# Kernel tuning notes

Hardware: AMD Instinct MI355X
Metric: run time of the kernel (lower is better)

Reference implementation:

```python
import jax, jax.numpy as jnp
import numpy as np

N_NODES = 50000
N_EDGES = 800000
HID = 128
HEADS = 1
VOCAB = 1001  # input_dim + 1
OUT = 16
NEG_SLOPE = 0.2  # DGL GATv2Conv default


def setup_inputs():
    key = jax.random.key(0)
    ks = jax.random.split(key, 12)
    s = 1.0 / np.sqrt(HID)
    inp = {}
    inp['feats'] = jax.random.randint(ks[0], (N_NODES, 2), 0, VOCAB, dtype=jnp.int64)
    inp['src'] = jax.random.randint(ks[1], (N_EDGES,), 0, N_NODES, dtype=jnp.int32)
    inp['dst'] = jax.random.randint(ks[2], (N_EDGES,), 0, N_NODES, dtype=jnp.int32)
    inp['key_emb'] = jax.random.normal(ks[3], (VOCAB, HID), jnp.float32)
    inp['val_emb'] = jax.random.normal(ks[4], (VOCAB, HID), jnp.float32)
    inp['W1'] = jax.random.uniform(ks[5], (HID, HEADS * HID), jnp.float32, -s, s)
    inp['attn1'] = jax.random.uniform(ks[6], (HEADS, HID), jnp.float32, -s, s)
    inp['W2'] = jax.random.uniform(ks[7], (HID, HEADS * HID), jnp.float32, -s, s)
    inp['attn2'] = jax.random.uniform(ks[8], (HEADS, HID), jnp.float32, -s, s)
    inp['cls_w'] = jax.random.uniform(ks[9], (HID, OUT), jnp.float32, -s, s)
    return inp


def _gatv2_layer(h, W, attn, src, dst):
    # share_weights=True: one linear transform for both src and dst roles
    feat = (h @ W).reshape(N_NODES, HEADS, HID)          # [N,H,D]
    e = jax.nn.leaky_relu(feat[src] + feat[dst], NEG_SLOPE)  # [E,H,D]
    logits = jnp.einsum('ehd,hd->eh', e, attn)            # [E,H]
    # segment softmax over incoming edges of each dst node
    m = jax.ops.segment_max(logits, dst, num_segments=N_NODES)  # [N,H]
    ex = jnp.exp(logits - m[dst])
    denom = jax.ops.segment_sum(ex, dst, num_segments=N_NODES)
    a = ex / denom[dst]                                   # [E,H]
    # weighted scatter-aggregate of src features to dst nodes
    return jax.ops.segment_sum(a[:, :, None] * feat[src], dst, num_segments=N_NODES)  # [N,H,D]


def reference(feats, src, dst, key_emb, val_emb, W1, attn1, W2, attn2, cls_w):
    h = jax.nn.relu(key_emb[feats[:, 0]] + val_emb[feats[:, 1]])  # [N,HID]
    h = _gatv2_layer(h, W1, attn1, src, dst).mean(axis=1)         # mean over heads
    h = _gatv2_layer(h, W2, attn2, src, dst).mean(axis=1)
    return h @ cls_w  # [N,OUT]
```

## Files before the change

kernel.cpp:

```cpp
#include <hip/hip_runtime.h>
#include <hip/hip_fp16.h>
#include <math.h>

#define HID 128

typedef _Float16 half8 __attribute__((ext_vector_type(8)));
typedef float floatx4 __attribute__((ext_vector_type(4)));

struct h4pack { __half2 a, b; };

__device__ __forceinline__ float4 h4tof4(h4pack h) {
  float2 lo = __half22float2(h.a);
  float2 hi = __half22float2(h.b);
  return make_float4(lo.x, lo.y, hi.x, hi.y);
}

__device__ __forceinline__ h4pack f4toh4(float4 v) {
  h4pack h;
  h.a = __floats2half2_rn(v.x, v.y);
  h.b = __floats2half2_rn(v.z, v.w);
  return h;
}

__global__ __launch_bounds__(256) void zero_kernel(int4* __restrict__ p, int n4) {
  int i = blockIdx.x * 256 + threadIdx.x;
  if (i < n4) p[i] = make_int4(0, 0, 0, 0);
}

__global__ __launch_bounds__(256) void hist_kernel(
    const int* __restrict__ dst, int* __restrict__ counts,
    int* __restrict__ rank, int E) {
  int e = blockIdx.x * 256 + threadIdx.x;
  if (e < E) rank[e] = atomicAdd(&counts[dst[e]], 1);
}

__global__ __launch_bounds__(256) void partial_kernel(
    const int* __restrict__ counts, int* __restrict__ partials, int N) {
  __shared__ int s[256];
  int idx = blockIdx.x * 256 + threadIdx.x;
  int c = (idx < N) ? counts[idx] : 0;
  s[threadIdx.x] = (idx < N) ? ((c + 7) & ~7) : 0;
  __syncthreads();
  for (int o = 128; o > 0; o >>= 1) {
    if (threadIdx.x < o) s[threadIdx.x] += s[threadIdx.x + o];
    __syncthreads();
  }
  if (threadIdx.x == 0) partials[blockIdx.x] = s[0];
}

__global__ __launch_bounds__(256) void scan2_kernel(
    const int* __restrict__ partials, int* __restrict__ bases, int NB) {
  __shared__ int s[256];
  int t = threadIdx.x;
  int v0 = (t < NB) ? partials[t] : 0;
  s[t] = v0;
  __syncthreads();
  for (int o = 1; o < 256; o <<= 1) {
    int v = (t >= o) ? s[t - o] : 0;
    __syncthreads();
    s[t] += v;
    __syncthreads();
  }
  bases[t] = s[t] - v0;
}

__global__ __launch_bounds__(256) void offs_kernel(
    const int* __restrict__ counts, const int* __restrict__ bases,
    int* __restrict__ offs, int* __restrict__ csr, int N) {
  __shared__ int s[256];
  int t = threadIdx.x;
  int idx = blockIdx.x * 256 + t;
  int deg = (idx < N) ? counts[idx] : 0;
  int c = (idx < N) ? ((deg + 7) & ~7) : 0;
  s[t] = c;
  __syncthreads();
  for (int o = 1; o < 256; o <<= 1) {
    int v = (t >= o) ? s[t - o] : 0;
    __syncthreads();
    s[t] += v;
    __syncthreads();
  }
  int base = bases[blockIdx.x];
  if (idx < N) {
    int o = base + s[t] - c;
    offs[idx] = o;
    for (int k = deg; k < c; ++k) csr[o + k] = 0;
  }
  if (idx == N - 1) offs[N] = base + s[t];
}

__global__ __launch_bounds__(256) void scatter_kernel(
    const int* __restrict__ src, const int* __restrict__ dst,
    const int* __restrict__ offs, const int* __restrict__ rank,
    int* __restrict__ csr, int E) {
  int e = blockIdx.x * 256 + threadIdx.x;
  if (e >= E) return;
  csr[offs[dst[e]] + rank[e]] = src[e];
}

__global__ __launch_bounds__(256) void embed_kernel(
    const int* __restrict__ feats, const float* __restrict__ ke,
    const float* __restrict__ ve, __half* __restrict__ h0, int N) {
  int gid = blockIdx.x * 256 + threadIdx.x;
  int n = gid >> 4, j = gid & 15;
  if (n >= N) return;
  int f0 = feats[2 * n], f1 = feats[2 * n + 1];
  const float4* a4 = (const float4*)(ke + (size_t)f0 * HID) + j * 2;
  const float4* b4 = (const float4*)(ve + (size_t)f1 * HID) + j * 2;
  float4 a0 = a4[0], a1 = a4[1], b0 = b4[0], b1 = b4[1];
  float4 v0, v1;
  v0.x = fmaxf(a0.x + b0.x, 0.f); v0.y = fmaxf(a0.y + b0.y, 0.f);
  v0.z = fmaxf(a0.z + b0.z, 0.f); v0.w = fmaxf(a0.w + b0.w, 0.f);
  v1.x = fmaxf(a1.x + b1.x, 0.f); v1.y = fmaxf(a1.y + b1.y, 0.f);
  v1.z = fmaxf(a1.z + b1.z, 0.f); v1.w = fmaxf(a1.w + b1.w, 0.f);
  h4pack* out = (h4pack*)h0 + (size_t)n * 32 + j * 2;
  out[0] = f4toh4(v0);
  out[1] = f4toh4(v1);
}

__global__ __launch_bounds__(256) void wprep_kernel(
    const float* __restrict__ W, __half* __restrict__ Wt) {
  int t = blockIdx.x * 256 + threadIdx.x;
  int k = t >> 7, c = t & 127;
  Wt[(size_t)c * HID + k] = __float2half(W[t]);
}

__global__ __launch_bounds__(256) void gemm_mfma_kernel(
    const __half* __restrict__ A, const __half* __restrict__ Wt,
    __half* __restrict__ F, int N) {
  int w = threadIdx.x >> 6;
  int lane = threadIdx.x & 63;
  int r = lane & 15, g = lane >> 4;
  int row0 = blockIdx.x * 64 + w * 16;
  if (row0 >= N) return;
  int arow = row0 + r;
  if (arow >= N) arow = N - 1;
  const half8* Ap = (const half8*)(A + (size_t)arow * HID + g * 8);
  half8 a0 = Ap[0];
  half8 a1 = Ap[4];
  half8 a2 = Ap[8];
  half8 a3 = Ap[12];
#pragma unroll
  for (int ct = 0; ct < 8; ++ct) {
    const half8* Bp = (const half8*)(Wt + (size_t)(ct * 16 + r) * HID + g * 8);
    half8 b0 = Bp[0], b1 = Bp[4], b2 = Bp[8], b3 = Bp[12];
    floatx4 c = {0.f, 0.f, 0.f, 0.f};
    c = __builtin_amdgcn_mfma_f32_16x16x32_f16(a0, b0, c, 0, 0, 0);
    c = __builtin_amdgcn_mfma_f32_16x16x32_f16(a1, b1, c, 0, 0, 0);
    c = __builtin_amdgcn_mfma_f32_16x16x32_f16(a2, b2, c, 0, 0, 0);
    c = __builtin_amdgcn_mfma_f32_16x16x32_f16(a3, b3, c, 0, 0, 0);
    int col = ct * 16 + r;
#pragma unroll
    for (int reg = 0; reg < 4; ++reg) {
      int row = row0 + g * 4 + reg;
      if (row < N) F[(size_t)row * HID + col] = __float2half(c[reg]);
    }
  }
}

__device__ __forceinline__ float dot4f(const float4& f, const float4& fd,
                                       const float4& a6, const float4& a4) {
  float t, p;
  t = f.x + fd.x; p = a6.x * t;         p = fmaf(a4.x, fabsf(t), p);
  t = f.y + fd.y; p = fmaf(a6.y, t, p); p = fmaf(a4.y, fabsf(t), p);
  t = f.z + fd.z; p = fmaf(a6.z, t, p); p = fmaf(a4.z, fabsf(t), p);
  t = f.w + fd.w; p = fmaf(a6.w, t, p); p = fmaf(a4.w, fabsf(t), p);
  return p;
}

__global__ __launch_bounds__(256) void gat_kernel(
    const __half* __restrict__ F, const int* __restrict__ offs,
    const int* __restrict__ counts, const int* __restrict__ csr,
    const float* __restrict__ attn, __half* __restrict__ Hout, int N) {
  int node = blockIdx.x * 8 + (threadIdx.x >> 5);
  if (node >= N) return;
  int q = threadIdx.x & 31;
  int lane = threadIdx.x & 63;
  const h4pack* F4h = (const h4pack*)F;
  float4 fd = h4tof4(F4h[(size_t)node * 32 + q]);
  float4 av = ((const float4*)attn)[q];
  float4 a6, a4;
  a6.x = 0.6f * av.x; a6.y = 0.6f * av.y; a6.z = 0.6f * av.z; a6.w = 0.6f * av.w;
  a4.x = 0.4f * av.x; a4.y = 0.4f * av.y; a4.z = 0.4f * av.z; a4.w = 0.4f * av.w;
  int ib = (lane & 32) << 2;
  bool b1 = (q & 1) != 0;
  bool b2 = (q & 2) != 0;
  bool b4 = (q & 4) != 0;

  int beg = offs[node];
  int cnt = counts[node];
  float l = 0.f;
  float4 acc = make_float4(0.f, 0.f, 0.f, 0.f);

  int nit = (cnt + 7) >> 3;
  const int* cp = csr + beg;
  for (int it = 0; it < nit; ++it) {
    const int4* qp = (const int4*)(cp + 8 * it);
    int4 sa = qp[0];
    int4 sb = qp[1];
    float4 fa0 = h4tof4(F4h[(size_t)sa.x * 32 + q]);
    float4 fa1 = h4tof4(F4h[(size_t)sa.y * 32 + q]);
    float4 fa2 = h4tof4(F4h[(size_t)sa.z * 32 + q]);
    float4 fa3 = h4tof4(F4h[(size_t)sa.w * 32 + q]);
    float4 fb0 = h4tof4(F4h[(size_t)sb.x * 32 + q]);
    float4 fb1 = h4tof4(F4h[(size_t)sb.y * 32 + q]);
    float4 fb2 = h4tof4(F4h[(size_t)sb.z * 32 + q]);
    float4 fb3 = h4tof4(F4h[(size_t)sb.w * 32 + q]);
    int rem = cnt - 8 * it;
    float p0 = dot4f(fa0, fd, a6, a4);
    float p1 = (1 < rem) ? dot4f(fa1, fd, a6, a4) : -INFINITY;
    float p2 = (2 < rem) ? dot4f(fa2, fd, a6, a4) : -INFINITY;
    float p3 = (3 < rem) ? dot4f(fa3, fd, a6, a4) : -INFINITY;
    float p4 = (4 < rem) ? dot4f(fb0, fd, a6, a4) : -INFINITY;
    float p5 = (5 < rem) ? dot4f(fb1, fd, a6, a4) : -INFINITY;
    float p6 = (6 < rem) ? dot4f(fb2, fd, a6, a4) : -INFINITY;
    float p7 = (7 < rem) ? dot4f(fb3, fd, a6, a4) : -INFINITY;
    float u0 = p0 + __shfl_xor(p0, 1, 64);
    float u1 = p1 + __shfl_xor(p1, 1, 64);
    float u2 = p2 + __shfl_xor(p2, 1, 64);
    float u3 = p3 + __shfl_xor(p3, 1, 64);
    float u4 = p4 + __shfl_xor(p4, 1, 64);
    float u5 = p5 + __shfl_xor(p5, 1, 64);
    float u6 = p6 + __shfl_xor(p6, 1, 64);
    float u7 = p7 + __shfl_xor(p7, 1, 64);
    float c0 = b1 ? u1 : u0;
    float c1 = b1 ? u3 : u2;
    float c2 = b1 ? u5 : u4;
    float c3 = b1 ? u7 : u6;
    float d0 = c0 + __shfl_xor(c0, 2, 64);
    float d1 = c1 + __shfl_xor(c1, 2, 64);
    float d2 = c2 + __shfl_xor(c2, 2, 64);
    float d3 = c3 + __shfl_xor(c3, 2, 64);
    float w0 = b2 ? d1 : d0;
    float w1 = b2 ? d3 : d2;
    float x0 = w0 + __shfl_xor(w0, 4, 64);
    float x1 = w1 + __shfl_xor(w1, 4, 64);
    float r = b4 ? x1 : x0;
    r += __shfl_xor(r, 8, 64);
    r += __shfl_xor(r, 16, 64);
    float ex = __expf(r);
    int exi = __float_as_int(ex);
    float e0 = __int_as_float(__builtin_amdgcn_ds_bpermute(ib +  0, exi));
    float e1 = __int_as_float(__builtin_amdgcn_ds_bpermute(ib +  4, exi));
    float e2 = __int_as_float(__builtin_amdgcn_ds_bpermute(ib +  8, exi));
    float e3 = __int_as_float(__builtin_amdgcn_ds_bpermute(ib + 12, exi));
    float e4 = __int_as_float(__builtin_amdgcn_ds_bpermute(ib + 16, exi));
    float e5 = __int_as_float(__builtin_amdgcn_ds_bpermute(ib + 20, exi));
    float e6 = __int_as_float(__builtin_amdgcn_ds_bpermute(ib + 24, exi));
    float e7 = __int_as_float(__builtin_amdgcn_ds_bpermute(ib + 28, exi));
    l += ((e0 + e1) + (e2 + e3)) + ((e4 + e5) + (e6 + e7));
    acc.x = fmaf(e0, fa0.x, acc.x); acc.x = fmaf(e1, fa1.x, acc.x);
    acc.x = fmaf(e2, fa2.x, acc.x); acc.x = fmaf(e3, fa3.x, acc.x);
    acc.x = fmaf(e4, fb0.x, acc.x); acc.x = fmaf(e5, fb1.x, acc.x);
    acc.x = fmaf(e6, fb2.x, acc.x); acc.x = fmaf(e7, fb3.x, acc.x);
    acc.y = fmaf(e0, fa0.y, acc.y); acc.y = fmaf(e1, fa1.y, acc.y);
    acc.y = fmaf(e2, fa2.y, acc.y); acc.y = fmaf(e3, fa3.y, acc.y);
    acc.y = fmaf(e4, fb0.y, acc.y); acc.y = fmaf(e5, fb1.y, acc.y);
    acc.y = fmaf(e6, fb2.y, acc.y); acc.y = fmaf(e7, fb3.y, acc.y);
    acc.z = fmaf(e0, fa0.z, acc.z); acc.z = fmaf(e1, fa1.z, acc.z);
    acc.z = fmaf(e2, fa2.z, acc.z); acc.z = fmaf(e3, fa3.z, acc.z);
    acc.z = fmaf(e4, fb0.z, acc.z); acc.z = fmaf(e5, fb1.z, acc.z);
    acc.z = fmaf(e6, fb2.z, acc.z); acc.z = fmaf(e7, fb3.z, acc.z);
    acc.w = fmaf(e0, fa0.w, acc.w); acc.w = fmaf(e1, fa1.w, acc.w);
    acc.w = fmaf(e2, fa2.w, acc.w); acc.w = fmaf(e3, fa3.w, acc.w);
    acc.w = fmaf(e4, fb0.w, acc.w); acc.w = fmaf(e5, fb1.w, acc.w);
    acc.w = fmaf(e6, fb2.w, acc.w); acc.w = fmaf(e7, fb3.w, acc.w);
  }
  float inv = (l > 0.f) ? 1.f / l : 0.f;
  acc.x *= inv; acc.y *= inv; acc.z *= inv; acc.w *= inv;
  ((h4pack*)Hout)[(size_t)node * 32 + q] = f4toh4(acc);
}

__global__ __launch_bounds__(256) void classify_kernel(
    const __half* __restrict__ H, const float* __restrict__ Wc,
    float* __restrict__ out, int N) {
  __shared__ float sW[HID * 16];
  __shared__ float sH[16][132];
  for (int i = threadIdx.x; i < HID * 16; i += 256) sW[i] = Wc[i];
  int row0 = blockIdx.x * 16;
  for (int i = threadIdx.x; i < 16 * 32; i += 256) {
    int r = i >> 5, j = i & 31;
    int row = row0 + r;
    float4 v = make_float4(0.f, 0.f, 0.f, 0.f);
    if (row < N) v = h4tof4(((const h4pack*)H)[(size_t)row * 32 + j]);
    ((float4*)&sH[r][0])[j] = v;
  }
  __syncthreads();
  int r = threadIdx.x >> 4;
  int c = threadIdx.x & 15;
  float acc = 0.f;
#pragma unroll 8
  for (int k = 0; k < HID; ++k) acc = fmaf(sH[r][k], sW[k * 16 + c], acc);
  int row = row0 + r;
  if (row < N) out[(size_t)row * 16 + c] = acc;
}

extern "C" void kernel_launch(void* const* d_in, const int* in_sizes, int n_in,
                              void* d_out, int out_size, void* d_ws, size_t ws_size,
                              hipStream_t stream) {
  const int* feats     = (const int*)d_in[0];
  const int* src       = (const int*)d_in[1];
  const int* dst       = (const int*)d_in[2];
  const float* key_emb = (const float*)d_in[3];
  const float* val_emb = (const float*)d_in[4];
  const float* W1      = (const float*)d_in[5];
  const float* attn1   = (const float*)d_in[6];
  const float* W2      = (const float*)d_in[7];
  const float* attn2   = (const float*)d_in[8];
  const float* cls_w   = (const float*)d_in[9];

  int N = in_sizes[0] / 2;
  int E = in_sizes[1];
  int NB = (N + 255) / 256;

  int Np = (N + 3) & ~3;
  int Ep = (E + 3) & ~3;
  char* ws = (char*)d_ws;
  __half* fbuf  = (__half*)ws;
  __half* hbuf  = (__half*)(ws + (size_t)Np * HID * 2);
  __half* ebuf  = (__half*)(ws + (size_t)Np * HID * 4);
  __half* Wt1   = (__half*)(ws + (size_t)Np * HID * 6);
  __half* Wt2   = Wt1 + HID * HID;
  int* counts   = (int*)(Wt2 + HID * HID);
  int* offs     = counts + Np;
  int* rank     = offs + Np + 4;
  int* csr      = rank + Ep;
  int* partials = csr + Ep + 8 * (size_t)Np;
  int* bases    = partials + 256;

  zero_kernel<<<(Np / 4 + 255) / 256, 256, 0, stream>>>((int4*)counts, Np / 4);

  hist_kernel<<<(E + 255) / 256, 256, 0, stream>>>(dst, counts, rank, E);
  partial_kernel<<<NB, 256, 0, stream>>>(counts, partials, N);
  scan2_kernel<<<1, 256, 0, stream>>>(partials, bases, NB);
  offs_kernel<<<NB, 256, 0, stream>>>(counts, bases, offs, csr, N);
  scatter_kernel<<<(E + 255) / 256, 256, 0, stream>>>(src, dst, offs, rank, csr, E);

  wprep_kernel<<<64, 256, 0, stream>>>(W1, Wt1);
  wprep_kernel<<<64, 256, 0, stream>>>(W2, Wt2);
  embed_kernel<<<((size_t)N * 16 + 255) / 256, 256, 0, stream>>>(
      feats, key_emb, val_emb, ebuf, N);

  int gblocks = (N + 63) / 64;
  gemm_mfma_kernel<<<gblocks, 256, 0, stream>>>(ebuf, Wt1, fbuf, N);
  gat_kernel<<<(N + 7) / 8, 256, 0, stream>>>(
      fbuf, offs, counts, csr, attn1, hbuf, N);
  gemm_mfma_kernel<<<gblocks, 256, 0, stream>>>(hbuf, Wt2, fbuf, N);
  gat_kernel<<<(N + 7) / 8, 256, 0, stream>>>(
      fbuf, offs, counts, csr, attn2, hbuf, N);

  classify_kernel<<<(N + 15) / 16, 256, 0, stream>>>(hbuf, cls_w, (float*)d_out, N);
}
```

Before: 205.4 us.

## Fuse embedding into first GEMM and collapse scan and weight-prep launches

The embedding lookup, add and ReLU are computed directly inside the first MFMA GEMM, so the fp16 embedding buffer is never written or read back. The three-kernel block scan that builds CSR offsets becomes one single-block scan of 1024 threads, and the two weight-transpose launches become one. This removes several launches and a full N×128 intermediate round trip through memory. The trade-offs are a serial per-thread loop of about 49 nodes inside one block for the scan, and gather loads from the embedding tables inside the GEMM.

```diff
diff --git a/kernel.cpp b/kernel.cpp
--- a/kernel.cpp
+++ b/kernel.cpp
@@ -34,59 +34,33 @@
   if (e < E) rank[e] = atomicAdd(&counts[dst[e]], 1);
 }
 
-__global__ __launch_bounds__(256) void partial_kernel(
-    const int* __restrict__ counts, int* __restrict__ partials, int N) {
-  __shared__ int s[256];
-  int idx = blockIdx.x * 256 + threadIdx.x;
-  int c = (idx < N) ? counts[idx] : 0;
-  s[threadIdx.x] = (idx < N) ? ((c + 7) & ~7) : 0;
+__global__ __launch_bounds__(1024) void scanoffs_kernel(
+    const int* __restrict__ counts, int* __restrict__ offs,
+    int* __restrict__ csr, int N) {
+  __shared__ int part[1024];
+  int t = threadIdx.x;
+  int chunk = (N + 1023) / 1024;
+  int start = t * chunk;
+  int end = min(start + chunk, N);
+  int s = 0;
+  for (int i = start; i < end; ++i) s += (counts[i] + 7) & ~7;
+  part[t] = s;
   __syncthreads();
-  for (int o = 128; o > 0; o >>= 1) {
-    if (threadIdx.x < o) s[threadIdx.x] += s[threadIdx.x + o];
+  for (int o = 1; o < 1024; o <<= 1) {
+    int v = (t >= o) ? part[t - o] : 0;
     __syncthreads();
-  }
-  if (threadIdx.x == 0) partials[blockIdx.x] = s[0];
-}
-
-__global__ __launch_bounds__(256) void scan2_kernel(
-    const int* __restrict__ partials, int* __restrict__ bases, int NB) {
-  __shared__ int s[256];
-  int t = threadIdx.x;
-  int v0 = (t < NB) ? partials[t] : 0;
-  s[t] = v0;
-  __syncthreads();
-  for (int o = 1; o < 256; o <<= 1) {
-    int v = (t >= o) ? s[t - o] : 0;
+    part[t] += v;
     __syncthreads();
-    s[t] += v;
-    __syncthreads();
-  }
-  bases[t] = s[t] - v0;
-}
-
-__global__ __launch_bounds__(256) void offs_kernel(
-    const int* __restrict__ counts, const int* __restrict__ bases,
-    int* __restrict__ offs, int* __restrict__ csr, int N) {
-  __shared__ int s[256];
-  int t = threadIdx.x;
-  int idx = blockIdx.x * 256 + t;
-  int deg = (idx < N) ? counts[idx] : 0;
-  int c = (idx < N) ? ((deg + 7) & ~7) : 0;
-  s[t] = c;
-  __syncthreads();
-  for (int o = 1; o < 256; o <<= 1) {
-    int v = (t >= o) ? s[t - o] : 0;
-    __syncthreads();
-    s[t] += v;
-    __syncthreads();
-  }
-  int base = bases[blockIdx.x];
-  if (idx < N) {
-    int o = base + s[t] - c;
-    offs[idx] = o;
-    for (int k = deg; k < c; ++k) csr[o + k] = 0;
-  }
-  if (idx == N - 1) offs[N] = base + s[t];
+  }
+  int run = (t > 0) ? part[t - 1] : 0;
+  for (int i = start; i < end; ++i) {
+    int deg = counts[i];
+    int c = (deg + 7) & ~7;
+    offs[i] = run;
+    for (int k = deg; k < c; ++k) csr[run + k] = 0;
+    run += c;
+  }
+  if (t == 1023) offs[N] = part[1023];
 }
 
 __global__ __launch_bounds__(256) void scatter_kernel(
@@ -98,36 +72,40 @@
   csr[offs[dst[e]] + rank[e]] = src[e];
 }
 
-__global__ __launch_bounds__(256) void embed_kernel(
-    const int* __restrict__ feats, const float* __restrict__ ke,
-    const float* __restrict__ ve, __half* __restrict__ h0, int N) {
-  int gid = blockIdx.x * 256 + threadIdx.x;
-  int n = gid >> 4, j = gid & 15;
-  if (n >= N) return;
-  int f0 = feats[2 * n], f1 = feats[2 * n + 1];
-  const float4* a4 = (const float4*)(ke + (size_t)f0 * HID) + j * 2;
-  const float4* b4 = (const float4*)(ve + (size_t)f1 * HID) + j * 2;
-  float4 a0 = a4[0], a1 = a4[1], b0 = b4[0], b1 = b4[1];
-  float4 v0, v1;
-  v0.x = fmaxf(a0.x + b0.x, 0.f); v0.y = fmaxf(a0.y + b0.y, 0.f);
-  v0.z = fmaxf(a0.z + b0.z, 0.f); v0.w = fmaxf(a0.w + b0.w, 0.f);
-  v1.x = fmaxf(a1.x + b1.x, 0.f); v1.y = fmaxf(a1.y + b1.y, 0.f);
-  v1.z = fmaxf(a1.z + b1.z, 0.f); v1.w = fmaxf(a1.w + b1.w, 0.f);
-  h4pack* out = (h4pack*)h0 + (size_t)n * 32 + j * 2;
-  out[0] = f4toh4(v0);
-  out[1] = f4toh4(v1);
-}
-
-__global__ __launch_bounds__(256) void wprep_kernel(
-    const float* __restrict__ W, __half* __restrict__ Wt) {
-  int t = blockIdx.x * 256 + threadIdx.x;
+__global__ __launch_bounds__(256) void wprep2_kernel(
+    const float* __restrict__ W1, const float* __restrict__ W2,
+    __half* __restrict__ Wt1, __half* __restrict__ Wt2) {
+  int b = blockIdx.x;
+  const float* W = (b < 64) ? W1 : W2;
+  __half* Wt = (b < 64) ? Wt1 : Wt2;
+  int t = (b & 63) * 256 + threadIdx.x;
   int k = t >> 7, c = t & 127;
   Wt[(size_t)c * HID + k] = __float2half(W[t]);
 }
 
+__device__ __forceinline__ half8 embed8(const float* __restrict__ kp,
+                                        const float* __restrict__ vp, int off) {
+  float4 k0 = *(const float4*)(kp + off);
+  float4 k1 = *(const float4*)(kp + off + 4);
+  float4 v0 = *(const float4*)(vp + off);
+  float4 v1 = *(const float4*)(vp + off + 4);
+  half8 h;
+  h[0] = (_Float16)fmaxf(k0.x + v0.x, 0.f);
+  h[1] = (_Float16)fmaxf(k0.y + v0.y, 0.f);
+  h[2] = (_Float16)fmaxf(k0.z + v0.z, 0.f);
+  h[3] = (_Float16)fmaxf(k0.w + v0.w, 0.f);
+  h[4] = (_Float16)fmaxf(k1.x + v1.x, 0.f);
+  h[5] = (_Float16)fmaxf(k1.y + v1.y, 0.f);
+  h[6] = (_Float16)fmaxf(k1.z + v1.z, 0.f);
+  h[7] = (_Float16)fmaxf(k1.w + v1.w, 0.f);
+  return h;
+}
+
+template <bool FUSE_EMBED>
 __global__ __launch_bounds__(256) void gemm_mfma_kernel(
-    const __half* __restrict__ A, const __half* __restrict__ Wt,
-    __half* __restrict__ F, int N) {
+    const __half* __restrict__ A, const int* __restrict__ feats,
+    const float* __restrict__ ke, const float* __restrict__ ve,
+    const __half* __restrict__ Wt, __half* __restrict__ F, int N) {
   int w = threadIdx.x >> 6;
   int lane = threadIdx.x & 63;
   int r = lane & 15, g = lane >> 4;
@@ -135,11 +113,22 @@
   if (row0 >= N) return;
   int arow = row0 + r;
   if (arow >= N) arow = N - 1;
-  const half8* Ap = (const half8*)(A + (size_t)arow * HID + g * 8);
-  half8 a0 = Ap[0];
-  half8 a1 = Ap[4];
-  half8 a2 = Ap[8];
-  half8 a3 = Ap[12];
+  half8 a0, a1, a2, a3;
+  if (FUSE_EMBED) {
+    int f0 = feats[2 * arow], f1 = feats[2 * arow + 1];
+    const float* kp = ke + (size_t)f0 * HID;
+    const float* vp = ve + (size_t)f1 * HID;
+    a0 = embed8(kp, vp, g * 8);
+    a1 = embed8(kp, vp, 32 + g * 8);
+    a2 = embed8(kp, vp, 64 + g * 8);
+    a3 = embed8(kp, vp, 96 + g * 8);
+  } else {
+    const half8* Ap = (const half8*)(A + (size_t)arow * HID + g * 8);
+    a0 = Ap[0];
+    a1 = Ap[4];
+    a2 = Ap[8];
+    a3 = Ap[12];
+  }
 #pragma unroll
   for (int ct = 0; ct < 8; ++ct) {
     const half8* Bp = (const half8*)(Wt + (size_t)(ct * 16 + r) * HID + g * 8);
@@ -311,42 +300,35 @@
 
   int N = in_sizes[0] / 2;
   int E = in_sizes[1];
-  int NB = (N + 255) / 256;
 
   int Np = (N + 3) & ~3;
   int Ep = (E + 3) & ~3;
   char* ws = (char*)d_ws;
   __half* fbuf  = (__half*)ws;
   __half* hbuf  = (__half*)(ws + (size_t)Np * HID * 2);
-  __half* ebuf  = (__half*)(ws + (size_t)Np * HID * 4);
-  __half* Wt1   = (__half*)(ws + (size_t)Np * HID * 6);
+  __half* Wt1   = (__half*)(ws + (size_t)Np * HID * 4);
   __half* Wt2   = Wt1 + HID * HID;
   int* counts   = (int*)(Wt2 + HID * HID);
   int* offs     = counts + Np;
   int* rank     = offs + Np + 4;
   int* csr      = rank + Ep;
-  int* partials = csr + Ep + 8 * (size_t)Np;
-  int* bases    = partials + 256;
 
   zero_kernel<<<(Np / 4 + 255) / 256, 256, 0, stream>>>((int4*)counts, Np / 4);
 
   hist_kernel<<<(E + 255) / 256, 256, 0, stream>>>(dst, counts, rank, E);
-  partial_kernel<<<NB, 256, 0, stream>>>(counts, partials, N);
-  scan2_kernel<<<1, 256, 0, stream>>>(partials, bases, NB);
-  offs_kernel<<<NB, 256, 0, stream>>>(counts, bases, offs, csr, N);
+  scanoffs_kernel<<<1, 1024, 0, stream>>>(counts, offs, csr, N);
   scatter_kernel<<<(E + 255) / 256, 256, 0, stream>>>(src, dst, offs, rank, csr, E);
-
-  wprep_kernel<<<64, 256, 0, stream>>>(W1, Wt1);
-  wprep_kernel<<<64, 256, 0, stream>>>(W2, Wt2);
-  embed_kernel<<<((size_t)N * 16 + 255) / 256, 256, 0, stream>>>(
-      feats, key_emb, val_emb, ebuf, N);
+  wprep2_kernel<<<128, 256, 0, stream>>>(W1, W2, Wt1, Wt2);
 
   int gblocks = (N + 63) / 64;
-  gemm_mfma_kernel<<<gblocks, 256, 0, stream>>>(ebuf, Wt1, fbuf, N);
-  gat_kernel<<<(N + 7) / 8, 256, 0, stream>>>(
+  int gatblocks = (N + 7) / 8;
+  gemm_mfma_kernel<true><<<gblocks, 256, 0, stream>>>(
+      nullptr, feats, key_emb, val_emb, Wt1, fbuf, N);
+  gat_kernel<<<gatblocks, 256, 0, stream>>>(
       fbuf, offs, counts, csr, attn1, hbuf, N);
-  gemm_mfma_kernel<<<gblocks, 256, 0, stream>>>(hbuf, Wt2, fbuf, N);
-  gat_kernel<<<(N + 7) / 8, 256, 0, stream>>>(
+  gemm_mfma_kernel<false><<<gblocks, 256, 0, stream>>>(
+      hbuf, nullptr, nullptr, nullptr, Wt2, fbuf, N);
+  gat_kernel<<<gatblocks, 256, 0, stream>>>(
       fbuf, offs, counts, csr, attn2, hbuf, N);
 
   classify_kernel<<<(N + 15) / 16, 256, 0, stream>>>(hbuf, cls_w, (float*)d_out, N);
```

Result: slower. 327.2 us (+59.3%).
